# Performance work log

Measured on AMD Instinct MI355X. Metric: run time of the kernel, lower is better.

## Reference

```python
import jax, jax.numpy as jnp
import numpy as np

M_Q = 32    # number of queries
N_G = 256   # number of gallery items
D = 128     # feature dim


def setup_inputs() -> dict:
    key = jax.random.key(0)
    k1, k2, k3 = jax.random.split(key, 3)
    qf = jax.random.uniform(k1, (M_Q, D), dtype=jnp.float32)
    x = jax.random.uniform(k2, (N_G, D), dtype=jnp.float32)
    Mp = jax.random.uniform(k3, (D, D), dtype=jnp.float32)
    ze = jnp.zeros((), dtype=jnp.float32)  # scalar clamp threshold
    return {"qf": qf, "x": x, "Mp": Mp, "ze": ze}


def reference(qf, x, Mp, ze):
    # qf: (m, d), x: (n, d), Mp: (d, d), ze: scalar
    u = jnp.maximum(qf[:, None, :], x[None, :, :])   # (m, n, d) elementwise max
    v = jnp.minimum(qf[:, None, :], x[None, :, :])   # (m, n, d) elementwise min
    # Jaccard-like similarity: sum(min) / sum(max)
    dist0 = v.sum(-1) / u.sum(-1)                    # (m, n)
    # Outer product u u^T per (i, j) pair, minus Mp, clamped at ze, summed over (d, d)
    outer = u[:, :, :, None] * u[:, :, None, :]      # (m, n, d, d)
    pen = jnp.maximum(ze, outer - Mp[None, None, :, :]).sum(axis=(-2, -1))  # (m, n)
    return dist0 - 0.001 * pen
```

## Files before the change

### kernel.cpp

```cpp
#include <hip/hip_runtime.h>
#include <hip/hip_bf16.h>

#define MQ 32
#define NG 256
#define DD 128

__device__ __forceinline__ float wred64(float v) {
    #pragma unroll
    for (int o = 32; o > 0; o >>= 1) v += __shfl_xor(v, o);
    return v;
}
__device__ __forceinline__ float hred32(float v) {
    #pragma unroll
    for (int o = 16; o > 0; o >>= 1) v += __shfl_xor(v, o);
    return v;
}

__global__ __launch_bounds__(256, 4)
void InferenceXtt_kernel(const float* __restrict__ qf,
                         const float* __restrict__ x,
                         const float* __restrict__ Mp,
                         const float* __restrict__ zep,
                         float* __restrict__ out) {
    __shared__ float u_T[DD * 12];
    __shared__ float su_sh[8], dist0_sh[8];
    __shared__ float pen_sh[4][8];
    __shared__ float msum_sh[4];

    const int t = threadIdx.x;
    const int w = t >> 6;
    const int l = t & 63;
    const int k = l & 31;
    const int d0 = k * 4;
    const int i  = blockIdx.x >> 5;
    const int j0 = (blockIdx.x & 31) * 8;

    const float ze = zep[0];

    {
        const int p = t >> 5;
        const float4 qv = *(const float4*)&qf[i * DD + d0];
        const float4 xv = *(const float4*)&x[(j0 + p) * DD + d0];
        const float ux = fmaxf(qv.x, xv.x), uy = fmaxf(qv.y, xv.y);
        const float uz = fmaxf(qv.z, xv.z), uw = fmaxf(qv.w, xv.w);
        const float vx = fminf(qv.x, xv.x), vy = fminf(qv.y, xv.y);
        const float vz = fminf(qv.z, xv.z), vw = fminf(qv.w, xv.w);
        u_T[(d0 + 0) * 12 + p] = ux;
        u_T[(d0 + 1) * 12 + p] = uy;
        u_T[(d0 + 2) * 12 + p] = uz;
        u_T[(d0 + 3) * 12 + p] = uw;
        const float su = hred32((ux + uy) + (uz + uw));
        const float sv = hred32((vx + vy) + (vz + vw));
        if (k == 0) { su_sh[p] = su; dist0_sh[p] = sv / su; }
    }

    float ub[8][4];
    {
        const float4 qv = *(const float4*)&qf[i * DD + d0];
        #pragma unroll
        for (int p = 0; p < 8; ++p) {
            const float4 xv = *(const float4*)&x[(j0 + p) * DD + d0];
            ub[p][0] = fmaxf(qv.x, xv.x);
            ub[p][1] = fmaxf(qv.y, xv.y);
            ub[p][2] = fmaxf(qv.z, xv.z);
            ub[p][3] = fmaxf(qv.w, xv.w);
        }
    }

    __syncthreads();

    float acc[8] = {0.f,0.f,0.f,0.f,0.f,0.f,0.f,0.f};
    float msum = 0.f;
    const int half = l >> 5;
    const float* mp_g = &Mp[(w * 32 + half) * DD + d0];
    const float* ua_g = &u_T[(w * 32 + half) * 12];
    #pragma unroll 2
    for (int s = 0; s < 16; ++s) {
        const float4 mp  = *(const float4*)mp_g;
        const float4 ua0 = *(const float4*)ua_g;
        const float4 ua1 = *(const float4*)(ua_g + 4);
        mp_g += 2 * DD;
        ua_g += 2 * 12;
        msum += (mp.x + mp.y) + (mp.z + mp.w);
        const float m0 = mp.x + ze, m1 = mp.y + ze;
        const float m2 = mp.z + ze, m3 = mp.w + ze;
        const float ua[8] = {ua0.x, ua0.y, ua0.z, ua0.w, ua1.x, ua1.y, ua1.z, ua1.w};
        #pragma unroll
        for (int p = 0; p < 8; ++p) {
            acc[p] += __builtin_fabsf(fmaf(ua[p], ub[p][0], -m0));
            acc[p] += __builtin_fabsf(fmaf(ua[p], ub[p][1], -m1));
            acc[p] += __builtin_fabsf(fmaf(ua[p], ub[p][2], -m2));
            acc[p] += __builtin_fabsf(fmaf(ua[p], ub[p][3], -m3));
        }
    }

    #pragma unroll
    for (int p = 0; p < 8; ++p) {
        const float S = wred64(acc[p]);
        if (l == p) pen_sh[w][p] = S;
    }
    const float ms = wred64(msum);
    if (l == 0) msum_sh[w] = ms;
    __syncthreads();

    if (t < 8) {
        const float S = (pen_sh[0][t] + pen_sh[1][t]) + (pen_sh[2][t] + pen_sh[3][t]);
        const float sumMp = (msum_sh[0] + msum_sh[1]) + (msum_sh[2] + msum_sh[3]);
        const float su = su_sh[t];
        const float pen = 8192.f * ze + 0.5f * (fmaf(su, su, -sumMp) + S);
        out[i * NG + j0 + t] = dist0_sh[t] - 0.001f * pen;
    }
}

extern "C" void kernel_launch(void* const* d_in, const int* in_sizes, int n_in,
                              void* d_out, int out_size, void* d_ws, size_t ws_size,
                              hipStream_t stream) {
    const float* qf = (const float*)d_in[0];
    const float* x  = (const float*)d_in[1];
    const float* Mp = (const float*)d_in[2];
    const float* ze = (const float*)d_in[3];
    float* out = (float*)d_out;
    InferenceXtt_kernel<<<dim3(MQ * 32), dim3(256), 0, stream>>>(qf, x, Mp, ze, out);
}
```

Before: 19.34 us.

## Split the d-row dimension across two blocks and combine with atomicAdd

Each (query, 8-gallery) tile is now handled by two blocks, each covering half of the Mp rows, which doubles the grid and halves the per-block loop trip count. Partial penalties are combined with atomicAdd into an output zeroed by a preceding hipMemsetAsync, and only the h==0 block adds the dist0 and su^2 terms. The aim is more parallelism and shorter per-block latency. The cost is an extra memset launch, atomics, and duplicated prologue work (loading x/qf and the reductions) in both halves.

```diff
diff --git a/kernel.cpp b/kernel.cpp
--- a/kernel.cpp
+++ b/kernel.cpp
@@ -16,13 +16,13 @@
     return v;
 }
 
-__global__ __launch_bounds__(256, 4)
+__global__ __launch_bounds__(256)
 void InferenceXtt_kernel(const float* __restrict__ qf,
                          const float* __restrict__ x,
                          const float* __restrict__ Mp,
                          const float* __restrict__ zep,
                          float* __restrict__ out) {
-    __shared__ float u_T[DD * 12];
+    __shared__ float u_T[64 * 12];
     __shared__ float su_sh[8], dist0_sh[8];
     __shared__ float pen_sh[4][8];
     __shared__ float msum_sh[4];
@@ -32,8 +32,12 @@
     const int l = t & 63;
     const int k = l & 31;
     const int d0 = k * 4;
-    const int i  = blockIdx.x >> 5;
-    const int j0 = (blockIdx.x & 31) * 8;
+    const int half = l >> 5;
+    const int bid = blockIdx.x;
+    const int i  = bid >> 6;
+    const int jg = (bid >> 1) & 31;
+    const int h  = bid & 1;
+    const int j0 = jg * 8;
 
     const float ze = zep[0];
 
@@ -45,10 +49,13 @@
         const float uz = fmaxf(qv.z, xv.z), uw = fmaxf(qv.w, xv.w);
         const float vx = fminf(qv.x, xv.x), vy = fminf(qv.y, xv.y);
         const float vz = fminf(qv.z, xv.z), vw = fminf(qv.w, xv.w);
-        u_T[(d0 + 0) * 12 + p] = ux;
-        u_T[(d0 + 1) * 12 + p] = uy;
-        u_T[(d0 + 2) * 12 + p] = uz;
-        u_T[(d0 + 3) * 12 + p] = uw;
+        const int r = d0 - h * 64;
+        if (r >= 0 && r < 64) {
+            u_T[(r + 0) * 12 + p] = ux;
+            u_T[(r + 1) * 12 + p] = uy;
+            u_T[(r + 2) * 12 + p] = uz;
+            u_T[(r + 3) * 12 + p] = uw;
+        }
         const float su = hred32((ux + uy) + (uz + uw));
         const float sv = hred32((vx + vy) + (vz + vw));
         if (k == 0) { su_sh[p] = su; dist0_sh[p] = sv / su; }
@@ -71,11 +78,10 @@
 
     float acc[8] = {0.f,0.f,0.f,0.f,0.f,0.f,0.f,0.f};
     float msum = 0.f;
-    const int half = l >> 5;
-    const float* mp_g = &Mp[(w * 32 + half) * DD + d0];
-    const float* ua_g = &u_T[(w * 32 + half) * 12];
+    const float* mp_g = &Mp[(h * 64 + w * 16 + half) * DD + d0];
+    const float* ua_g = &u_T[(w * 16 + half) * 12];
     #pragma unroll 2
-    for (int s = 0; s < 16; ++s) {
+    for (int s = 0; s < 8; ++s) {
         const float4 mp  = *(const float4*)mp_g;
         const float4 ua0 = *(const float4*)ua_g;
         const float4 ua1 = *(const float4*)(ua_g + 4);
@@ -104,11 +110,14 @@
     __syncthreads();
 
     if (t < 8) {
-        const float S = (pen_sh[0][t] + pen_sh[1][t]) + (pen_sh[2][t] + pen_sh[3][t]);
-        const float sumMp = (msum_sh[0] + msum_sh[1]) + (msum_sh[2] + msum_sh[3]);
-        const float su = su_sh[t];
-        const float pen = 8192.f * ze + 0.5f * (fmaf(su, su, -sumMp) + S);
-        out[i * NG + j0 + t] = dist0_sh[t] - 0.001f * pen;
+        const float S_h  = (pen_sh[0][t] + pen_sh[1][t]) + (pen_sh[2][t] + pen_sh[3][t]);
+        const float ms_h = (msum_sh[0] + msum_sh[1]) + (msum_sh[2] + msum_sh[3]);
+        float part = -0.0005f * (S_h - ms_h);
+        if (h == 0) {
+            const float su = su_sh[t];
+            part += dist0_sh[t] - 0.001f * (8192.f * ze + 0.5f * su * su);
+        }
+        atomicAdd(&out[i * NG + j0 + t], part);
     }
 }
 
@@ -120,5 +129,6 @@
     const float* Mp = (const float*)d_in[2];
     const float* ze = (const float*)d_in[3];
     float* out = (float*)d_out;
-    InferenceXtt_kernel<<<dim3(MQ * 32), dim3(256), 0, stream>>>(qf, x, Mp, ze, out);
+    hipMemsetAsync(out, 0, (size_t)out_size * sizeof(float), stream);
+    InferenceXtt_kernel<<<dim3(MQ * 32 * 2), dim3(256), 0, stream>>>(qf, x, Mp, ze, out);
 }
```

New measurement: 25.62 us. 1.32x slower.

## Use packed fp16 math with Mp staged in shared memory

Applied to the files above, without the earlier changes.

Each block now converts Mp to fp16 (negated and offset by ze), stores the whole 128x128 matrix in shared memory, and stores u in half2 layouts. The inner penalty loop then runs on packed half2 FMA, abs and add, processing two elements per instruction, with accumulators kept in fp16. The aim is to double ALU throughput and drop repeated fp32 global loads of Mp. In exchange there is fp16 rounding and fp16 accumulation error, and about 32KB of extra shared memory per block, which can lower occupancy.

```diff
diff --git a/kernel.cpp b/kernel.cpp
--- a/kernel.cpp
+++ b/kernel.cpp
@@ -1,5 +1,5 @@
 #include <hip/hip_runtime.h>
-#include <hip/hip_bf16.h>
+#include <hip/hip_fp16.h>
 
 #define MQ 32
 #define NG 256
@@ -16,21 +16,19 @@
     return v;
 }
 
-__global__ __launch_bounds__(256, 4)
+__global__ __launch_bounds__(256)
 void InferenceXtt_kernel(const float* __restrict__ qf,
                          const float* __restrict__ x,
                          const float* __restrict__ Mp,
                          const float* __restrict__ zep,
                          float* __restrict__ out) {
-    __shared__ float u_T[DD * 12];
-    __shared__ float su_sh[8], dist0_sh[8];
-    __shared__ float pen_sh[4][8];
-    __shared__ float msum_sh[4];
+    __shared__ __half  negm_sh[DD * DD];
+    __shared__ __half2 ua_sh[DD][8];
+    __shared__ __half2 ucp_sh[DD / 2][8];
+    __shared__ float suh_sh[8], dist0_sh[8], pen_sh[4][8], msum_sh[4];
 
     const int t = threadIdx.x;
-    const int w = t >> 6;
-    const int l = t & 63;
-    const int k = l & 31;
+    const int w = t >> 6, l = t & 63, k = l & 31, half = l >> 5;
     const int d0 = k * 4;
     const int i  = blockIdx.x >> 5;
     const int j0 = (blockIdx.x & 31) * 8;
@@ -41,73 +39,95 @@
         const int p = t >> 5;
         const float4 qv = *(const float4*)&qf[i * DD + d0];
         const float4 xv = *(const float4*)&x[(j0 + p) * DD + d0];
-        const float ux = fmaxf(qv.x, xv.x), uy = fmaxf(qv.y, xv.y);
-        const float uz = fmaxf(qv.z, xv.z), uw = fmaxf(qv.w, xv.w);
-        const float vx = fminf(qv.x, xv.x), vy = fminf(qv.y, xv.y);
-        const float vz = fminf(qv.z, xv.z), vw = fminf(qv.w, xv.w);
-        u_T[(d0 + 0) * 12 + p] = ux;
-        u_T[(d0 + 1) * 12 + p] = uy;
-        u_T[(d0 + 2) * 12 + p] = uz;
-        u_T[(d0 + 3) * 12 + p] = uw;
-        const float su = hred32((ux + uy) + (uz + uw));
-        const float sv = hred32((vx + vy) + (vz + vw));
-        if (k == 0) { su_sh[p] = su; dist0_sh[p] = sv / su; }
+        const float u0 = fmaxf(qv.x, xv.x), u1 = fmaxf(qv.y, xv.y);
+        const float u2 = fmaxf(qv.z, xv.z), u3 = fmaxf(qv.w, xv.w);
+        const float v0 = fminf(qv.x, xv.x), v1 = fminf(qv.y, xv.y);
+        const float v2 = fminf(qv.z, xv.z), v3 = fminf(qv.w, xv.w);
+        const __half h0 = __float2half(u0), h1 = __float2half(u1);
+        const __half h2 = __float2half(u2), h3 = __float2half(u3);
+        ua_sh[d0 + 0][p] = __half2half2(h0);
+        ua_sh[d0 + 1][p] = __half2half2(h1);
+        ua_sh[d0 + 2][p] = __half2half2(h2);
+        ua_sh[d0 + 3][p] = __half2half2(h3);
+        ucp_sh[k * 2 + 0][p] = __halves2half2(h0, h1);
+        ucp_sh[k * 2 + 1][p] = __halves2half2(h2, h3);
+        const float suh = hred32((__half2float(h0) + __half2float(h1)) +
+                                 (__half2float(h2) + __half2float(h3)));
+        const float su  = hred32((u0 + u1) + (u2 + u3));
+        const float sv  = hred32((v0 + v1) + (v2 + v3));
+        if (k == 0) { suh_sh[p] = suh; dist0_sh[p] = sv / su; }
     }
 
-    float ub[8][4];
     {
-        const float4 qv = *(const float4*)&qf[i * DD + d0];
+        float ms = 0.f;
+        const float4* g = (const float4*)Mp;
+        #pragma unroll 4
+        for (int r = 0; r < 16; ++r) {
+            const int f = t + r * 256;
+            const float4 v = g[f];
+            union { __half2 h[2]; uint2 u; } pk;
+            pk.h[0] = __floats2half2_rn(-(v.x + ze), -(v.y + ze));
+            pk.h[1] = __floats2half2_rn(-(v.z + ze), -(v.w + ze));
+            *(uint2*)&negm_sh[4 * f] = pk.u;
+            ms += (__low2float(pk.h[0]) + __high2float(pk.h[0]))
+                + (__low2float(pk.h[1]) + __high2float(pk.h[1]));
+        }
+        ms = wred64(ms);
+        if (l == 0) msum_sh[w] = ms;
+    }
+    __syncthreads();
+
+    __half2 ub2[8][2];
+    #pragma unroll
+    for (int cg = 0; cg < 2; ++cg) {
+        union { uint4 u; __half2 h[4]; } A, B;
+        A.u = *(const uint4*)&ucp_sh[k * 2 + cg][0];
+        B.u = *(const uint4*)&ucp_sh[k * 2 + cg][4];
+        #pragma unroll
+        for (int p = 0; p < 4; ++p) { ub2[p][cg] = A.h[p]; ub2[p + 4][cg] = B.h[p]; }
+    }
+
+    __half2 acc2[8][2];
+    #pragma unroll
+    for (int p = 0; p < 8; ++p)
+        acc2[p][0] = acc2[p][1] = __floats2half2_rn(0.f, 0.f);
+
+    const __half*  mrow  = &negm_sh[(w * 32 + half) * DD + d0];
+    const __half2* uarow = &ua_sh[w * 32 + half][0];
+    #pragma unroll 4
+    for (int s = 0; s < 16; ++s) {
+        union { uint2 u; __half2 h[2]; } M;
+        M.u = *(const uint2*)mrow;
+        union { uint4 u; __half2 h[4]; } A, B;
+        A.u = *(const uint4*)uarow;
+        B.u = *(const uint4*)(uarow + 4);
+        mrow  += 2 * DD;
+        uarow += 2 * 8;
         #pragma unroll
         for (int p = 0; p < 8; ++p) {
-            const float4 xv = *(const float4*)&x[(j0 + p) * DD + d0];
-            ub[p][0] = fmaxf(qv.x, xv.x);
-            ub[p][1] = fmaxf(qv.y, xv.y);
-            ub[p][2] = fmaxf(qv.z, xv.z);
-            ub[p][3] = fmaxf(qv.w, xv.w);
-        }
-    }
-
-    __syncthreads();
-
-    float acc[8] = {0.f,0.f,0.f,0.f,0.f,0.f,0.f,0.f};
-    float msum = 0.f;
-    const int half = l >> 5;
-    const float* mp_g = &Mp[(w * 32 + half) * DD + d0];
-    const float* ua_g = &u_T[(w * 32 + half) * 12];
-    #pragma unroll 2
-    for (int s = 0; s < 16; ++s) {
-        const float4 mp  = *(const float4*)mp_g;
-        const float4 ua0 = *(const float4*)ua_g;
-        const float4 ua1 = *(const float4*)(ua_g + 4);
-        mp_g += 2 * DD;
-        ua_g += 2 * 12;
-        msum += (mp.x + mp.y) + (mp.z + mp.w);
-        const float m0 = mp.x + ze, m1 = mp.y + ze;
-        const float m2 = mp.z + ze, m3 = mp.w + ze;
-        const float ua[8] = {ua0.x, ua0.y, ua0.z, ua0.w, ua1.x, ua1.y, ua1.z, ua1.w};
-        #pragma unroll
-        for (int p = 0; p < 8; ++p) {
-            acc[p] += __builtin_fabsf(fmaf(ua[p], ub[p][0], -m0));
-            acc[p] += __builtin_fabsf(fmaf(ua[p], ub[p][1], -m1));
-            acc[p] += __builtin_fabsf(fmaf(ua[p], ub[p][2], -m2));
-            acc[p] += __builtin_fabsf(fmaf(ua[p], ub[p][3], -m3));
+            const __half2 ua2 = (p < 4) ? A.h[p] : B.h[p - 4];
+            const __half2 w01 = __hfma2(ua2, ub2[p][0], M.h[0]);
+            const __half2 w23 = __hfma2(ua2, ub2[p][1], M.h[1]);
+            acc2[p][0] = __hadd2(acc2[p][0], __habs2(w01));
+            acc2[p][1] = __hadd2(acc2[p][1], __habs2(w23));
         }
     }
 
     #pragma unroll
     for (int p = 0; p < 8; ++p) {
-        const float S = wred64(acc[p]);
-        if (l == p) pen_sh[w][p] = S;
+        const float S = (__low2float(acc2[p][0]) + __high2float(acc2[p][0]))
+                      + (__low2float(acc2[p][1]) + __high2float(acc2[p][1]));
+        const float Sr = wred64(S);
+        if (l == p) pen_sh[w][p] = Sr;
     }
-    const float ms = wred64(msum);
-    if (l == 0) msum_sh[w] = ms;
     __syncthreads();
 
     if (t < 8) {
-        const float S = (pen_sh[0][t] + pen_sh[1][t]) + (pen_sh[2][t] + pen_sh[3][t]);
-        const float sumMp = (msum_sh[0] + msum_sh[1]) + (msum_sh[2] + msum_sh[3]);
-        const float su = su_sh[t];
-        const float pen = 8192.f * ze + 0.5f * (fmaf(su, su, -sumMp) + S);
+        float S = 0.f, msneg = 0.f;
+        #pragma unroll
+        for (int ww = 0; ww < 4; ++ww) { S += pen_sh[ww][t]; msneg += msum_sh[ww]; }
+        const float suh = suh_sh[t];
+        const float pen = 16384.f * ze + 0.5f * (fmaf(suh, suh, msneg) + S);
         out[i * NG + j0 + t] = dist0_sh[t] - 0.001f * pen;
     }
 }
```

Measured after the change: 19.08 us. No clear change (-1.3%).
